# Kernel optimization log

Measured on AMD Instinct MI355X. Metric: run time of the kernel, lower is better.

Reference implementation:

```python
import jax, jax.numpy as jnp
import numpy as np

N, E, P = 100000, 1600000, 10000
NODE_DIM, EDGE_DIM, H = 128, 64, 64


def setup_inputs() -> dict:
    key = jax.random.key(0)
    ks = jax.random.split(key, 12)
    inp = {
        "node_features": jax.random.normal(ks[0], (N, NODE_DIM), dtype=jnp.float32),
        "edge_index": jax.random.randint(ks[1], (2, E), 0, N, dtype=jnp.int64),
        "edge_attr": jax.random.normal(ks[2], (E, EDGE_DIM), dtype=jnp.float32),
        "post_idx": jax.random.randint(ks[3], (P,), 0, N, dtype=jnp.int64),
        # parameters (torch Linear convention: W is [out, in])
        "W_node": jax.random.normal(ks[4], (H, NODE_DIM), dtype=jnp.float32) * 0.05,
        "b_node": jax.random.normal(ks[5], (H,), dtype=jnp.float32) * 0.05,
        "W_edge": jax.random.normal(ks[6], (H, EDGE_DIM), dtype=jnp.float32) * 0.05,
        "b_edge": jax.random.normal(ks[7], (H,), dtype=jnp.float32) * 0.05,
        "W_conv": jax.random.normal(ks[8], (H, 2 * H), dtype=jnp.float32) * 0.05,
        "b_conv": jax.random.normal(ks[9], (H,), dtype=jnp.float32) * 0.05,
        "W_out": jax.random.normal(ks[10], (1, H), dtype=jnp.float32) * 0.05,
        "b_out": jax.random.normal(ks[11], (1,), dtype=jnp.float32) * 0.05,
    }
    return inp


def reference(node_features, edge_index, edge_attr, post_idx,
              W_node, b_node, W_edge, b_edge, W_conv, b_conv, W_out, b_out):
    # Encode nodes and edges: relu(Linear(.))
    node_emb = jax.nn.relu(node_features @ W_node.T + b_node)   # [N, H]
    edge_emb = jax.nn.relu(edge_attr @ W_edge.T + b_edge)       # [E, H]

    src, dst = edge_index[0], edge_index[1]
    # Per-edge message: conv(concat(node_emb[src], edge_emb)) with bias,
    # equivalent to split-matmul to avoid materializing the [E, 2H] concat.
    Wc_node, Wc_edge = W_conv[:, :H], W_conv[:, H:]
    msg = node_emb[src] @ Wc_node.T + edge_emb @ Wc_edge.T + b_conv  # [E, H]

    # Scatter-add into destination nodes (bias added once per incoming edge,
    # matching the torch per-edge loop semantics).
    messages = jax.ops.segment_sum(msg, dst, num_segments=node_emb.shape[0])

    node_emb = node_emb + messages
    post_emb = node_emb[post_idx]                                # [P, H]
    logits = (post_emb @ W_out.T + b_out).squeeze(-1)            # [P]
    return jax.nn.sigmoid(logits)
```

## Files before the change

kernel.cpp:

```cpp
#include <hip/hip_runtime.h>
#include <hip/hip_bf16.h>
#include <math.h>

#define N_NODES 100000
#define N_EDGES 1600000
#define N_POSTS 10000
#define ND 128
#define H 64
#define SCAN_B 1024
#define SCAN_NB ((N_NODES + SCAN_B - 1) / SCAN_B)

typedef __attribute__((ext_vector_type(8))) short bf16x8;
typedef __attribute__((ext_vector_type(4))) float f32x4;

static __device__ __forceinline__ unsigned short f2bf(float f) {
  return __builtin_bit_cast(unsigned short, __float2bfloat16(f));
}

static __device__ __forceinline__ bf16x8 pack8(const float* v) {
  bf16x8 r;
#pragma unroll
  for (int i = 0; i < 8; ++i) r[i] = (short)f2bf(v[i]);
  return r;
}

__device__ __forceinline__ float bcastf(float v, int lane) {
  return __builtin_bit_cast(float, __builtin_amdgcn_readlane(__builtin_bit_cast(int, v), lane));
}

__device__ __forceinline__ int load_idx(const void* p, long long i, int is64) {
  if (is64) return (int)((const long long*)p)[i];
  return ((const int*)p)[i];
}

static __device__ __forceinline__ int imin(int a, int b) { return a < b ? a : b; }

__global__ void init_kernel(const void* __restrict__ eidx, int* __restrict__ cnt2,
                            int* __restrict__ flag) {
  int i = blockIdx.x * blockDim.x + threadIdx.x;
  if (i < 2 * N_NODES) cnt2[i] = 0;
  if (blockIdx.x == 0 && threadIdx.x < 64) {
    int v = ((const int*)eidx)[2 * threadIdx.x + 1];
    unsigned long long b = __ballot(v != 0);
    if (threadIdx.x == 0) flag[0] = (b == 0ULL) ? 1 : 0;
  }
}

__global__ void mark_kernel(const void* __restrict__ pidx, int* __restrict__ pf,
                            const int* __restrict__ flag) {
  const int is64 = flag[0];
  int i = blockIdx.x * blockDim.x + threadIdx.x;
  if (i < N_POSTS) pf[load_idx(pidx, i, is64)] = 1;
}

__global__ void hist_kernel(const void* __restrict__ eidx, int* __restrict__ cnt,
                            const int* __restrict__ pf, const int* __restrict__ flag) {
  const int is64 = flag[0];
  int i = blockIdx.x * blockDim.x + threadIdx.x;
  const int stride = gridDim.x * blockDim.x;
  for (; i < N_EDGES; i += stride) {
    int d = load_idx(eidx, (long long)N_EDGES + i, is64);
    if (pf[d]) atomicAdd(&cnt[d], 1);
  }
}

__global__ void __launch_bounds__(SCAN_B) scan_block_kernel(int* __restrict__ cnt,
                                                            int* __restrict__ btot) {
  __shared__ int wsum[16];
  const int i = blockIdx.x * SCAN_B + threadIdx.x;
  const int lane = threadIdx.x & 63;
  const int wv = threadIdx.x >> 6;
  const int x = (i < N_NODES) ? cnt[i] : 0;
  int s = x;
#pragma unroll
  for (int off = 1; off < 64; off <<= 1) {
    int y = __shfl_up(s, off, 64);
    if (lane >= off) s += y;
  }
  if (lane == 63) wsum[wv] = s;
  __syncthreads();
  if (wv == 0) {
    int t = (lane < 16) ? wsum[lane] : 0;
#pragma unroll
    for (int off = 1; off < 16; off <<= 1) {
      int y = __shfl_up(t, off, 64);
      if (lane >= off) t += y;
    }
    if (lane < 16) wsum[lane] = t;
  }
  __syncthreads();
  const int woff = (wv == 0) ? 0 : wsum[wv - 1];
  if (i < N_NODES) cnt[i] = woff + s - x;
  if (threadIdx.x == 0) btot[blockIdx.x] = wsum[15];
}

__global__ void __launch_bounds__(SCAN_B) scan_add_kernel(int* __restrict__ cnt,
                                                          const int* __restrict__ btot,
                                                          int* __restrict__ Mp) {
  __shared__ int buf[128];
  if (threadIdx.x < 128) buf[threadIdx.x] = (threadIdx.x < SCAN_NB) ? btot[threadIdx.x] : 0;
  __syncthreads();
#pragma unroll
  for (int off = 1; off < 128; off <<= 1) {
    int y = 0;
    if (threadIdx.x < 128 && threadIdx.x >= off) y = buf[threadIdx.x - off];
    __syncthreads();
    if (threadIdx.x < 128) buf[threadIdx.x] += y;
    __syncthreads();
  }
  const int i = blockIdx.x * SCAN_B + threadIdx.x;
  const int excl = (blockIdx.x == 0) ? 0 : buf[blockIdx.x - 1];
  if (i < N_NODES) cnt[i] += excl;
  if (blockIdx.x == 0 && threadIdx.x == 0) Mp[0] = buf[SCAN_NB - 1];
}

__global__ void scatter_kernel(const void* __restrict__ eidx, int* __restrict__ ofs,
                               const int* __restrict__ pf, int4* __restrict__ eS,
                               const int* __restrict__ flag) {
  const int is64 = flag[0];
  int i = blockIdx.x * blockDim.x + threadIdx.x;
  const int stride = gridDim.x * blockDim.x;
  for (; i < N_EDGES; i += stride) {
    int d = load_idx(eidx, (long long)N_EDGES + i, is64);
    if (pf[d]) {
      int s = load_idx(eidx, i, is64);
      int pos = atomicAdd(&ofs[d], 1);
      eS[pos] = make_int4(i, s, d, 0);
    }
  }
}

__global__ void __launch_bounds__(256, 2) node_kernel_mfma(
    const float* __restrict__ nf, const float* __restrict__ Wn,
    const float* __restrict__ bn, const float* __restrict__ Wc,
    const float* __restrict__ bc, const int* __restrict__ pf,
    float* __restrict__ acc, float* __restrict__ T2) {
  __shared__ float lds[4][64 * 17];
  __shared__ __attribute__((aligned(16))) float bshn[64];
  __shared__ __attribute__((aligned(16))) float bshc[64];
  const int lane = threadIdx.x & 63;
  const int wslot = threadIdx.x >> 6;
  float* myl = lds[wslot];
  const int wid = blockIdx.x * 4 + wslot;
  const int nw = gridDim.x * 4;
  const int e16 = lane & 15;
  const int g = lane >> 4;

  if (threadIdx.x < 64) {
    bshn[threadIdx.x] = bn[threadIdx.x];
    bshc[threadIdx.x] = bc[threadIdx.x];
  }

  bf16x8 wN[4][4], wC1[4][2];
#pragma unroll
  for (int mt = 0; mt < 4; ++mt) {
#pragma unroll
    for (int t = 0; t < 4; ++t) {
      float tmp[8];
      const float* rowA = Wn + (mt * 16 + e16) * ND + t * 32 + g * 4;
      *(f32x4*)(tmp) = *(const f32x4*)(rowA);
      *(f32x4*)(tmp + 4) = *(const f32x4*)(rowA + 16);
      wN[mt][t] = pack8(tmp);
    }
#pragma unroll
    for (int t = 0; t < 2; ++t) {
      float tmp[8];
      const float* rowC = Wc + (mt * 16 + e16) * (2 * H) + t * 32 + g * 4;
      *(f32x4*)(tmp) = *(const f32x4*)(rowC);
      *(f32x4*)(tmp + 4) = *(const f32x4*)(rowC + 16);
      wC1[mt][t] = pack8(tmp);
    }
  }
  __syncthreads();

  const int NTN = N_NODES / 16;
  for (int tile = wid; tile < NTN; tile += nw) {
    const int n0 = tile * 16;
    const float* base = nf + (long long)(n0 + e16) * ND;

    bf16x8 b1[4];
#pragma unroll
    for (int t = 0; t < 4; ++t) {
      float tmp[8];
      *(f32x4*)(tmp) = *(const f32x4*)(base + t * 32 + g * 4);
      *(f32x4*)(tmp + 4) = *(const f32x4*)(base + t * 32 + 16 + g * 4);
      b1[t] = pack8(tmp);
    }

    f32x4 d1[4];
#pragma unroll
    for (int mt = 0; mt < 4; ++mt) d1[mt] = *(const f32x4*)(bshn + mt * 16 + g * 4);
#pragma unroll
    for (int t = 0; t < 4; ++t)
#pragma unroll
      for (int mt = 0; mt < 4; ++mt)
        d1[mt] = __builtin_amdgcn_mfma_f32_16x16x32_bf16(wN[mt][t], b1[t], d1[mt], 0, 0, 0);

#pragma unroll
    for (int mt = 0; mt < 4; ++mt)
#pragma unroll
      for (int r = 0; r < 4; ++r) d1[mt][r] = fmaxf(d1[mt][r], 0.f);

    bf16x8 b2[2];
#pragma unroll
    for (int t = 0; t < 2; ++t) {
      float tmp[8];
#pragma unroll
      for (int i = 0; i < 4; ++i) {
        tmp[i] = d1[2 * t][i];
        tmp[4 + i] = d1[2 * t + 1][i];
      }
      b2[t] = pack8(tmp);
    }

    f32x4 d2[4];
#pragma unroll
    for (int mt = 0; mt < 4; ++mt) d2[mt] = *(const f32x4*)(bshc + mt * 16 + g * 4);
#pragma unroll
    for (int t = 0; t < 2; ++t)
#pragma unroll
      for (int mt = 0; mt < 4; ++mt)
        d2[mt] = __builtin_amdgcn_mfma_f32_16x16x32_bf16(wC1[mt][t], b2[t], d2[mt], 0, 0, 0);

    const unsigned long long pmask = __ballot(lane < 16 && pf[n0 + lane] != 0);

#pragma unroll
    for (int mt = 0; mt < 4; ++mt)
#pragma unroll
      for (int r = 0; r < 4; ++r)
        myl[(mt * 16 + g * 4 + r) * 17 + e16] = d1[mt][r];
#pragma unroll
    for (int e = 0; e < 16; ++e)
      if ((pmask >> e) & 1)
        acc[(long long)(n0 + e) * H + lane] = myl[lane * 17 + e];

#pragma unroll
    for (int mt = 0; mt < 4; ++mt)
#pragma unroll
      for (int r = 0; r < 4; ++r)
        myl[(mt * 16 + g * 4 + r) * 17 + e16] = d2[mt][r];
#pragma unroll
    for (int e = 0; e < 16; ++e)
      T2[(long long)(n0 + e) * H + lane] = myl[lane * 17 + e];
  }
}

__global__ void __launch_bounds__(256, 2) edge_kernel_sorted(
    const float* __restrict__ ea, const float* __restrict__ We,
    const float* __restrict__ be, const float* __restrict__ Wc,
    const float* __restrict__ T2, float* __restrict__ acc,
    const int4* __restrict__ eS, const int* __restrict__ Mp) {
  __shared__ float lds[4][64 * 17];
  __shared__ __attribute__((aligned(16))) float bsh[64];
  const int lane = threadIdx.x & 63;
  const int wslot = threadIdx.x >> 6;
  float* myl = lds[wslot];
  const int wid = blockIdx.x * 4 + wslot;
  const int nw = gridDim.x * 4;
  const int e16 = lane & 15;
  const int g = lane >> 4;

  if (threadIdx.x < 64) bsh[threadIdx.x] = be[threadIdx.x];

  bf16x8 wA[4][2], wC[4][2];
#pragma unroll
  for (int mt = 0; mt < 4; ++mt) {
#pragma unroll
    for (int t = 0; t < 2; ++t) {
      float tmp[8];
      const float* rowA = We + (mt * 16 + e16) * H + t * 32 + g * 4;
      *(f32x4*)(tmp) = *(const f32x4*)(rowA);
      *(f32x4*)(tmp + 4) = *(const f32x4*)(rowA + 16);
      wA[mt][t] = pack8(tmp);
      const float* rowC = Wc + (mt * 16 + e16) * (2 * H) + H + t * 32 + g * 4;
      *(f32x4*)(tmp) = *(const f32x4*)(rowC);
      *(f32x4*)(tmp + 4) = *(const f32x4*)(rowC + 16);
      wC[mt][t] = pack8(tmp);
    }
  }
  __syncthreads();

  const int M = Mp[0];
  const int ntiles = (M + 15) >> 4;
  const int chunk = (ntiles + nw - 1) / nw;
  const int t0 = wid * chunk;
  const int t1 = imin(t0 + chunk, ntiles);
  if (t0 >= t1) return;

  int4 eC = make_int4(0, 0, 0, 0);
  {
    const int i0 = t0 * 16 + e16;
    if (i0 < M) eC = eS[i0];
  }
  f32x4 eaC[4];
  {
    const float* base = ea + (long long)eC.x * H;
    eaC[0] = *(const f32x4*)(base + g * 4);
    eaC[1] = *(const f32x4*)(base + 16 + g * 4);
    eaC[2] = *(const f32x4*)(base + 32 + g * 4);
    eaC[3] = *(const f32x4*)(base + 48 + g * 4);
  }
  int4 eN = eC;
  if (t0 + 1 < t1) {
    const int i1 = (t0 + 1) * 16 + e16;
    eN = (i1 < M) ? eS[i1] : make_int4(0, 0, 0, 0);
  }

  int run_d = -1;
  float run_v = 0.f;

  for (int tile = t0; tile < t1; ++tile) {
    bf16x8 b1[2];
#pragma unroll
    for (int t = 0; t < 2; ++t) {
      float tmp[8];
#pragma unroll
      for (int i = 0; i < 4; ++i) {
        tmp[i] = eaC[t * 2][i];
        tmp[4 + i] = eaC[t * 2 + 1][i];
      }
      b1[t] = pack8(tmp);
    }
    const int srcc = eC.y;
    const int dstc = eC.z;

    if (tile + 1 < t1) {
      const float* base = ea + (long long)eN.x * H;
      eaC[0] = *(const f32x4*)(base + g * 4);
      eaC[1] = *(const f32x4*)(base + 16 + g * 4);
      eaC[2] = *(const f32x4*)(base + 32 + g * 4);
      eaC[3] = *(const f32x4*)(base + 48 + g * 4);
    }
    eC = eN;
    if (tile + 2 < t1) {
      const int i2 = (tile + 2) * 16 + e16;
      eN = (i2 < M) ? eS[i2] : make_int4(0, 0, 0, 0);
    }

    f32x4 d1[4];
#pragma unroll
    for (int mt = 0; mt < 4; ++mt) d1[mt] = *(const f32x4*)(bsh + mt * 16 + g * 4);
#pragma unroll
    for (int t = 0; t < 2; ++t)
#pragma unroll
      for (int mt = 0; mt < 4; ++mt)
        d1[mt] = __builtin_amdgcn_mfma_f32_16x16x32_bf16(wA[mt][t], b1[t], d1[mt], 0, 0, 0);

    bf16x8 b2[2];
#pragma unroll
    for (int t = 0; t < 2; ++t) {
      float tmp[8];
#pragma unroll
      for (int i = 0; i < 4; ++i) {
        tmp[i] = fmaxf(d1[2 * t][i], 0.f);
        tmp[4 + i] = fmaxf(d1[2 * t + 1][i], 0.f);
      }
      b2[t] = pack8(tmp);
    }

#pragma unroll
    for (int mt = 0; mt < 4; ++mt) {
      f32x4 d2 = (f32x4){0.f, 0.f, 0.f, 0.f};
      d2 = __builtin_amdgcn_mfma_f32_16x16x32_bf16(wC[mt][0], b2[0], d2, 0, 0, 0);
      d2 = __builtin_amdgcn_mfma_f32_16x16x32_bf16(wC[mt][1], b2[1], d2, 0, 0, 0);
#pragma unroll
      for (int r = 0; r < 4; ++r)
        myl[(mt * 16 + g * 4 + r) * 17 + e16] = d2[r];
    }

    const int nval = imin(16, M - tile * 16);
#pragma unroll
    for (int half = 0; half < 2; ++half) {
      float mv[8];
#pragma unroll
      for (int e = 0; e < 8; ++e) {
        const int s = __builtin_amdgcn_readlane(srcc, half * 8 + e);
        mv[e] = myl[lane * 17 + half * 8 + e] + T2[(long long)s * H + lane];
      }
      const int hi = imin(8, nval - half * 8);
      for (int e = 0; e < hi; ++e) {
        const int d = __builtin_amdgcn_readlane(dstc, half * 8 + e);
        if (d != run_d) {
          if (run_d >= 0) atomicAdd(&acc[(long long)run_d * H + lane], run_v);
          run_d = d;
          run_v = mv[e];
        } else {
          run_v += mv[e];
        }
      }
    }
  }
  if (run_d >= 0) atomicAdd(&acc[(long long)run_d * H + lane], run_v);
}

__global__ void __launch_bounds__(256, 2) node_kernel(
    const float* __restrict__ nf, const float* __restrict__ Wn,
    const float* __restrict__ bn, const float* __restrict__ Wc,
    const float* __restrict__ bc, float* __restrict__ acc,
    float* __restrict__ T2) {
  const int lane = threadIdx.x & 63;
  const int wid = blockIdx.x * (blockDim.x >> 6) + (threadIdx.x >> 6);
  const int nw = gridDim.x * (blockDim.x >> 6);

  float wn[ND];
#pragma unroll
  for (int i = 0; i < ND / 4; ++i) {
    float4 v = ((const float4*)(Wn + lane * ND))[i];
    wn[4 * i] = v.x; wn[4 * i + 1] = v.y; wn[4 * i + 2] = v.z; wn[4 * i + 3] = v.w;
  }
  float wc[H];
#pragma unroll
  for (int i = 0; i < H / 4; ++i) {
    float4 v = ((const float4*)(Wc + lane * 2 * H))[i];
    wc[4 * i] = v.x; wc[4 * i + 1] = v.y; wc[4 * i + 2] = v.z; wc[4 * i + 3] = v.w;
  }
  const float bnl = bn[lane];
  const float bcl = bc[lane];

  for (int n = wid; n < N_NODES; n += nw) {
    const float xa = nf[(long long)n * ND + lane];
    const float xb = nf[(long long)n * ND + 64 + lane];
    float a0 = 0.f, a1 = 0.f, a2 = 0.f, a3 = 0.f;
#pragma unroll
    for (int k = 0; k < 64; k += 4) {
      a0 = fmaf(bcastf(xa, k + 0), wn[k + 0], a0);
      a1 = fmaf(bcastf(xa, k + 1), wn[k + 1], a1);
      a2 = fmaf(bcastf(xa, k + 2), wn[k + 2], a2);
      a3 = fmaf(bcastf(xa, k + 3), wn[k + 3], a3);
    }
#pragma unroll
    for (int k = 0; k < 64; k += 4) {
      a0 = fmaf(bcastf(xb, k + 0), wn[64 + k + 0], a0);
      a1 = fmaf(bcastf(xb, k + 1), wn[64 + k + 1], a1);
      a2 = fmaf(bcastf(xb, k + 2), wn[64 + k + 2], a2);
      a3 = fmaf(bcastf(xb, k + 3), wn[64 + k + 3], a3);
    }
    float e = fmaxf(a0 + a1 + a2 + a3 + bnl, 0.f);

    float t0 = 0.f, t1 = 0.f, t2 = 0.f, t3 = 0.f;
#pragma unroll
    for (int j = 0; j < 64; j += 4) {
      t0 = fmaf(bcastf(e, j + 0), wc[j + 0], t0);
      t1 = fmaf(bcastf(e, j + 1), wc[j + 1], t1);
      t2 = fmaf(bcastf(e, j + 2), wc[j + 2], t2);
      t3 = fmaf(bcastf(e, j + 3), wc[j + 3], t3);
    }
    float t = t0 + t1 + t2 + t3 + bcl;

    acc[(long long)n * H + lane] = e;
    T2[(long long)n * H + lane] = t;
  }
}

__global__ void __launch_bounds__(256, 2) edge_kernel(
    const void* __restrict__ eidx, const float* __restrict__ ea,
    const float* __restrict__ We, const float* __restrict__ be,
    const float* __restrict__ Wc, const float* __restrict__ T2,
    float* __restrict__ acc, const int* __restrict__ flag) {
  __shared__ float lds[4][64 * 17];
  const int lane = threadIdx.x & 63;
  const int wslot = threadIdx.x >> 6;
  float* myl = lds[wslot];
  const int wid = blockIdx.x * 4 + wslot;
  const int nw = gridDim.x * 4;
  const int is64 = flag[0];
  const int e16 = lane & 15;
  const int g = lane >> 4;
  const int NT = N_EDGES / 16;

  bf16x8 wA[4][2], wC[4][2];
#pragma unroll
  for (int mt = 0; mt < 4; ++mt) {
#pragma unroll
    for (int t = 0; t < 2; ++t) {
      float tmp[8];
      const float* rowA = We + (mt * 16 + e16) * H + t * 32 + g * 4;
      *(f32x4*)(tmp) = *(const f32x4*)(rowA);
      *(f32x4*)(tmp + 4) = *(const f32x4*)(rowA + 16);
      wA[mt][t] = pack8(tmp);
      const float* rowC = Wc + (mt * 16 + e16) * (2 * H) + H + t * 32 + g * 4;
      *(f32x4*)(tmp) = *(const f32x4*)(rowC);
      *(f32x4*)(tmp + 4) = *(const f32x4*)(rowC + 16);
      wC[mt][t] = pack8(tmp);
    }
  }
  f32x4 bias[4];
#pragma unroll
  for (int mt = 0; mt < 4; ++mt)
#pragma unroll
    for (int r = 0; r < 4; ++r) bias[mt][r] = be[mt * 16 + g * 4 + r];

  f32x4 ean[4];
  int srcn = 0, dstn = 0;
  int tile = wid;
  if (tile < NT) {
    const float* base = ea + (long long)(tile * 16 + e16) * H;
#pragma unroll
    for (int t = 0; t < 2; ++t) {
      ean[t * 2] = *(const f32x4*)(base + t * 32 + g * 4);
      ean[t * 2 + 1] = *(const f32x4*)(base + t * 32 + 16 + g * 4);
    }
    srcn = load_idx(eidx, (long long)tile * 16 + e16, is64);
    dstn = load_idx(eidx, (long long)N_EDGES + (long long)tile * 16 + e16, is64);
  }

  for (; tile < NT; tile += nw) {
    f32x4 eac[4];
#pragma unroll
    for (int i = 0; i < 4; ++i) eac[i] = ean[i];
    const int srcc = srcn, dstc = dstn;

    const int tn = tile + nw;
    if (tn < NT) {
      const float* base = ea + (long long)(tn * 16 + e16) * H;
#pragma unroll
      for (int t = 0; t < 2; ++t) {
        ean[t * 2] = *(const f32x4*)(base + t * 32 + g * 4);
        ean[t * 2 + 1] = *(const f32x4*)(base + t * 32 + 16 + g * 4);
      }
      srcn = load_idx(eidx, (long long)tile * 16 + e16 + nw * 16, is64);
      dstn = load_idx(eidx, (long long)N_EDGES + (long long)tn * 16 + e16, is64);
    }

    bf16x8 b1[2];
#pragma unroll
    for (int t = 0; t < 2; ++t) {
      float tmp[8];
#pragma unroll
      for (int i = 0; i < 4; ++i) {
        tmp[i] = eac[t * 2][i];
        tmp[4 + i] = eac[t * 2 + 1][i];
      }
      b1[t] = pack8(tmp);
    }

    f32x4 d1[4];
#pragma unroll
    for (int mt = 0; mt < 4; ++mt) d1[mt] = bias[mt];
#pragma unroll
    for (int t = 0; t < 2; ++t)
#pragma unroll
      for (int mt = 0; mt < 4; ++mt)
        d1[mt] = __builtin_amdgcn_mfma_f32_16x16x32_bf16(wA[mt][t], b1[t], d1[mt], 0, 0, 0);

    bf16x8 b2[2];
#pragma unroll
    for (int t = 0; t < 2; ++t) {
      float tmp[8];
#pragma unroll
      for (int i = 0; i < 4; ++i) {
        tmp[i] = fmaxf(d1[2 * t][i], 0.f);
        tmp[4 + i] = fmaxf(d1[2 * t + 1][i], 0.f);
      }
      b2[t] = pack8(tmp);
    }

    f32x4 d2[4];
#pragma unroll
    for (int mt = 0; mt < 4; ++mt) d2[mt] = (f32x4){0.f, 0.f, 0.f, 0.f};
#pragma unroll
    for (int t = 0; t < 2; ++t)
#pragma unroll
      for (int mt = 0; mt < 4; ++mt)
        d2[mt] = __builtin_amdgcn_mfma_f32_16x16x32_bf16(wC[mt][t], b2[t], d2[mt], 0, 0, 0);

#pragma unroll
    for (int mt = 0; mt < 4; ++mt)
#pragma unroll
      for (int r = 0; r < 4; ++r)
        myl[(mt * 16 + g * 4 + r) * 17 + e16] = d2[mt][r];

#pragma unroll
    for (int e = 0; e < 16; ++e) {
      const int s = __builtin_amdgcn_readlane(srcc, e);
      const int d = __builtin_amdgcn_readlane(dstc, e);
      const float m = myl[lane * 17 + e] + T2[(long long)s * H + lane];
      atomicAdd(&acc[(long long)d * H + lane], m);
    }
  }
}

__global__ void __launch_bounds__(256) out_kernel(
    const void* __restrict__ pidx, const float* __restrict__ acc,
    const float* __restrict__ Wo, const float* __restrict__ bo,
    float* __restrict__ out, const int* __restrict__ flag) {
  const int lane = threadIdx.x & 63;
  const int w = blockIdx.x * (blockDim.x >> 6) + (threadIdx.x >> 6);
  if (w >= N_POSTS) return;
  const int is64 = flag[0];
  const int idx = load_idx(pidx, w, is64);
  float v = acc[(long long)idx * H + lane] * Wo[lane];
#pragma unroll
  for (int s = 32; s > 0; s >>= 1) v += __shfl_xor(v, s, 64);
  if (lane == 0) {
    float logit = v + bo[0];
    out[w] = 1.f / (1.f + expf(-logit));
  }
}

extern "C" void kernel_launch(void* const* d_in, const int* in_sizes, int n_in,
                              void* d_out, int out_size, void* d_ws, size_t ws_size,
                              hipStream_t stream) {
  const float* nf = (const float*)d_in[0];
  const void* eidx = d_in[1];
  const float* ea = (const float*)d_in[2];
  const void* pidx = d_in[3];
  const float* Wn = (const float*)d_in[4];
  const float* bn = (const float*)d_in[5];
  const float* We = (const float*)d_in[6];
  const float* be = (const float*)d_in[7];
  const float* Wc = (const float*)d_in[8];
  const float* bc = (const float*)d_in[9];
  const float* Wo = (const float*)d_in[10];
  const float* bo = (const float*)d_in[11];
  float* out = (float*)d_out;

  float* acc = (float*)d_ws;
  float* T2 = acc + (size_t)N_NODES * H;
  int4* eS = (int4*)(T2 + (size_t)N_NODES * H);
  int* cnt = (int*)(eS + N_EDGES);
  int* pf = cnt + N_NODES;
  int* btot = pf + N_NODES;
  int* Mp = btot + 128;
  int* flag = Mp + 1;

  const size_t need_sorted = (size_t)2 * N_NODES * H * 4 + (size_t)N_EDGES * 16 +
                             (size_t)2 * N_NODES * 4 + 128 * 4 + 8;

  if (ws_size >= need_sorted) {
    init_kernel<<<(2 * N_NODES + 255) / 256, 256, 0, stream>>>(eidx, cnt, flag);
    mark_kernel<<<(N_POSTS + 255) / 256, 256, 0, stream>>>(pidx, pf, flag);
    hist_kernel<<<2048, 256, 0, stream>>>(eidx, cnt, pf, flag);
    scan_block_kernel<<<SCAN_NB, SCAN_B, 0, stream>>>(cnt, btot);
    scan_add_kernel<<<SCAN_NB, SCAN_B, 0, stream>>>(cnt, btot, Mp);
    scatter_kernel<<<2048, 256, 0, stream>>>(eidx, cnt, pf, eS, flag);
    node_kernel_mfma<<<512, 256, 0, stream>>>(nf, Wn, bn, Wc, bc, pf, acc, T2);
    edge_kernel_sorted<<<1024, 256, 0, stream>>>(ea, We, be, Wc, T2, acc, eS, Mp);
    out_kernel<<<(N_POSTS + 3) / 4, 256, 0, stream>>>(pidx, acc, Wo, bo, out, flag);
  } else {
    int* flag2 = (int*)(T2 + (size_t)N_NODES * H);
    init_kernel<<<1, 256, 0, stream>>>(eidx, flag2 - 1, flag2);
    node_kernel<<<1024, 256, 0, stream>>>(nf, Wn, bn, Wc, bc, acc, T2);
    edge_kernel<<<1024, 256, 0, stream>>>(eidx, ea, We, be, Wc, T2, acc, flag2);
    out_kernel<<<(N_POSTS + 3) / 4, 256, 0, stream>>>(pidx, acc, Wo, bo, out, flag2);
  }
}
```

Baseline: 109.4 us.

## Compact post-relevant edges during histogram so scatter reads only compacted list

```diff
diff --git a/kernel.cpp b/kernel.cpp
--- a/kernel.cpp
+++ b/kernel.cpp
@@ -38,7 +38,7 @@
 __global__ void init_kernel(const void* __restrict__ eidx, int* __restrict__ cnt2,
                             int* __restrict__ flag) {
   int i = blockIdx.x * blockDim.x + threadIdx.x;
-  if (i < 2 * N_NODES) cnt2[i] = 0;
+  if (i < 2 * N_NODES + 1) cnt2[i] = 0;
   if (blockIdx.x == 0 && threadIdx.x < 64) {
     int v = ((const int*)eidx)[2 * threadIdx.x + 1];
     unsigned long long b = __ballot(v != 0);
@@ -53,14 +53,21 @@
   if (i < N_POSTS) pf[load_idx(pidx, i, is64)] = 1;
 }
 
-__global__ void hist_kernel(const void* __restrict__ eidx, int* __restrict__ cnt,
-                            const int* __restrict__ pf, const int* __restrict__ flag) {
+__global__ void compact_hist_kernel(const void* __restrict__ eidx,
+                                    const int* __restrict__ pf, int* __restrict__ cnt,
+                                    int4* __restrict__ cT, int* __restrict__ Mc,
+                                    const int* __restrict__ flag) {
   const int is64 = flag[0];
   int i = blockIdx.x * blockDim.x + threadIdx.x;
   const int stride = gridDim.x * blockDim.x;
   for (; i < N_EDGES; i += stride) {
     int d = load_idx(eidx, (long long)N_EDGES + i, is64);
-    if (pf[d]) atomicAdd(&cnt[d], 1);
+    if (pf[d]) {
+      int s = load_idx(eidx, i, is64);
+      atomicAdd(&cnt[d], 1);
+      int pos = atomicAdd(Mc, 1);
+      cT[pos] = make_int4(i, s, d, 0);
+    }
   }
 }
 
@@ -95,8 +102,7 @@
 }
 
 __global__ void __launch_bounds__(SCAN_B) scan_add_kernel(int* __restrict__ cnt,
-                                                          const int* __restrict__ btot,
-                                                          int* __restrict__ Mp) {
+                                                          const int* __restrict__ btot) {
   __shared__ int buf[128];
   if (threadIdx.x < 128) buf[threadIdx.x] = (threadIdx.x < SCAN_NB) ? btot[threadIdx.x] : 0;
   __syncthreads();
@@ -111,22 +117,17 @@
   const int i = blockIdx.x * SCAN_B + threadIdx.x;
   const int excl = (blockIdx.x == 0) ? 0 : buf[blockIdx.x - 1];
   if (i < N_NODES) cnt[i] += excl;
-  if (blockIdx.x == 0 && threadIdx.x == 0) Mp[0] = buf[SCAN_NB - 1];
-}
-
-__global__ void scatter_kernel(const void* __restrict__ eidx, int* __restrict__ ofs,
-                               const int* __restrict__ pf, int4* __restrict__ eS,
-                               const int* __restrict__ flag) {
-  const int is64 = flag[0];
+}
+
+__global__ void scatter_kernel(const int4* __restrict__ cT, int* __restrict__ ofs,
+                               int4* __restrict__ eS, const int* __restrict__ Mc) {
+  const int M = Mc[0];
   int i = blockIdx.x * blockDim.x + threadIdx.x;
   const int stride = gridDim.x * blockDim.x;
-  for (; i < N_EDGES; i += stride) {
-    int d = load_idx(eidx, (long long)N_EDGES + i, is64);
-    if (pf[d]) {
-      int s = load_idx(eidx, i, is64);
-      int pos = atomicAdd(&ofs[d], 1);
-      eS[pos] = make_int4(i, s, d, 0);
-    }
+  for (; i < M; i += stride) {
+    int4 t = cT[i];
+    int pos = atomicAdd(&ofs[t.z], 1);
+    eS[pos] = t;
   }
 }
 
@@ -518,7 +519,7 @@
         ean[t * 2] = *(const f32x4*)(base + t * 32 + g * 4);
         ean[t * 2 + 1] = *(const f32x4*)(base + t * 32 + 16 + g * 4);
       }
-      srcn = load_idx(eidx, (long long)tile * 16 + e16 + nw * 16, is64);
+      srcn = load_idx(eidx, (long long)tn * 16 + e16, is64);
       dstn = load_idx(eidx, (long long)N_EDGES + (long long)tn * 16 + e16, is64);
     }
 
@@ -618,24 +619,25 @@
   float* acc = (float*)d_ws;
   float* T2 = acc + (size_t)N_NODES * H;
   int4* eS = (int4*)(T2 + (size_t)N_NODES * H);
-  int* cnt = (int*)(eS + N_EDGES);
+  int4* cT = eS + N_EDGES;
+  int* cnt = (int*)(cT + N_EDGES);
   int* pf = cnt + N_NODES;
-  int* btot = pf + N_NODES;
-  int* Mp = btot + 128;
-  int* flag = Mp + 1;
-
-  const size_t need_sorted = (size_t)2 * N_NODES * H * 4 + (size_t)N_EDGES * 16 +
-                             (size_t)2 * N_NODES * 4 + 128 * 4 + 8;
+  int* Mc = pf + N_NODES;
+  int* btot = Mc + 1;
+  int* flag = btot + 128;
+
+  const size_t need_sorted = (size_t)2 * N_NODES * H * 4 + (size_t)2 * N_EDGES * 16 +
+                             (size_t)2 * N_NODES * 4 + 4 + 128 * 4 + 4;
 
   if (ws_size >= need_sorted) {
-    init_kernel<<<(2 * N_NODES + 255) / 256, 256, 0, stream>>>(eidx, cnt, flag);
+    init_kernel<<<(2 * N_NODES + 256) / 256, 256, 0, stream>>>(eidx, cnt, flag);
     mark_kernel<<<(N_POSTS + 255) / 256, 256, 0, stream>>>(pidx, pf, flag);
-    hist_kernel<<<2048, 256, 0, stream>>>(eidx, cnt, pf, flag);
+    compact_hist_kernel<<<2048, 256, 0, stream>>>(eidx, pf, cnt, cT, Mc, flag);
     scan_block_kernel<<<SCAN_NB, SCAN_B, 0, stream>>>(cnt, btot);
-    scan_add_kernel<<<SCAN_NB, SCAN_B, 0, stream>>>(cnt, btot, Mp);
-    scatter_kernel<<<2048, 256, 0, stream>>>(eidx, cnt, pf, eS, flag);
+    scan_add_kernel<<<SCAN_NB, SCAN_B, 0, stream>>>(cnt, btot);
+    scatter_kernel<<<512, 256, 0, stream>>>(cT, cnt, eS, Mc);
     node_kernel_mfma<<<512, 256, 0, stream>>>(nf, Wn, bn, Wc, bc, pf, acc, T2);
-    edge_kernel_sorted<<<1024, 256, 0, stream>>>(ea, We, be, Wc, T2, acc, eS, Mp);
+    edge_kernel_sorted<<<512, 256, 0, stream>>>(ea, We, be, Wc, T2, acc, eS, Mc);
     out_kernel<<<(N_POSTS + 3) / 4, 256, 0, stream>>>(pidx, acc, Wo, bo, out, flag);
   } else {
     int* flag2 = (int*)(T2 + (size_t)N_NODES * H);
```

Result: slower. 378.9 us (+246.3%).
